# Optimization experiments

Measured on AMD Instinct MI355X. Metric: run time of the kernel, lower is better.

The kernel has to match this reference:

```python
import jax, jax.numpy as jnp
import numpy as np

B, N, D, H = 2, 2048, 1024, 16
Dh = D // H
SCALE = Dh ** -0.5


def setup_inputs() -> dict:
    key = jax.random.key(0)
    ks = jax.random.split(key, 5)
    init = lambda k, sh, fan: (jax.random.normal(k, sh, jnp.float32) / np.sqrt(fan)).astype(jnp.float32)
    return {
        "x": jax.random.normal(ks[0], (B, N, D), jnp.float32),
        "w_qkv": init(ks[1], (D, 3 * D), D),   # to_qkv (no bias)
        "w_hkv": init(ks[2], (D, 2 * D), D),   # hkv_processor: Linear(dim, 2*dim), split -> HK, HV
        "w_out": init(ks[3], (D, D), D),       # to_out weight
        "b_out": jnp.zeros((D,), jnp.float32), # to_out bias
        "alpha": jnp.ones((1, H, 1, 1), jnp.float32),
    }


def _split_heads(t):  # (B,N,D) -> (B,H,N,Dh)
    return t.reshape(B, N, H, Dh).transpose(0, 2, 1, 3)


def _rope(x, theta=10000.0):
    # lucidrains rotary_embedding_torch: interleaved pairs (x[2i], x[2i+1])
    n, dh = x.shape[-2], x.shape[-1]
    freqs = 1.0 / (theta ** (jnp.arange(0, dh, 2, dtype=jnp.float32) / dh))
    ang = jnp.arange(n, dtype=jnp.float32)[:, None] * freqs          # (N, Dh/2)
    cos = jnp.repeat(jnp.cos(ang), 2, axis=-1)                        # (N, Dh)
    sin = jnp.repeat(jnp.sin(ang), 2, axis=-1)
    xp = x.reshape(*x.shape[:-1], dh // 2, 2)
    xrot = jnp.stack((-xp[..., 1], xp[..., 0]), axis=-1).reshape(x.shape)
    return x * cos + xrot * sin


def reference(x, w_qkv, w_hkv, w_out, b_out, alpha):
    q, k, v = (_split_heads(t) for t in jnp.split(x @ w_qkv, 3, axis=-1))
    hk, hv = (_split_heads(t) for t in jnp.split(x @ w_hkv, 2, axis=-1))
    q = _rope(q)
    k = _rope(k)

    qk = jnp.einsum('bhnd,bhmd->bhnm', q, k) * SCALE          # (B,H,N,N)
    hkk = jnp.einsum('bhnd,bhmd->bhnm', hk, k)                # (B,H,N,N)
    qhk = jnp.sum(q * hk, axis=-1, keepdims=True)             # (B,H,N,1)
    scores = qk - jax.nn.silu(hkk * qhk * SCALE)

    mask = jnp.tril(jnp.ones((N, N), dtype=bool))
    scores = jnp.where(mask, scores, -jnp.inf)
    W = jax.nn.softmax(scores, axis=-1)

    hvv = jnp.einsum('bhnd,bhmd->bhnm', hv, v)                # (B,H,N,N)
    mod = jnp.sum(hvv * W, axis=-1, keepdims=True)            # (B,H,N,1)
    o = jnp.einsum('bhnm,bhmd->bhnd', W, v) - jax.nn.sigmoid(alpha) * mod * hv

    attn_out = o.transpose(0, 2, 1, 3).reshape(B, N, D)
    return attn_out @ w_out + b_out
```

## Files before the change

### kernel.cpp

```cpp
#include <hip/hip_runtime.h>
#include <math.h>

typedef unsigned int u32;
typedef unsigned short u16;
typedef __attribute__((ext_vector_type(4))) float f32x4;
typedef __attribute__((ext_vector_type(8))) short s16x8;

#define BB 2
#define NN 2048
#define DD 1024
#define HH 16
#define ROWS 4096
#define QC 5120
#define SCALE 0.125f
#define LOG2E 1.44269504088896f
#define SC2 (SCALE * LOG2E)

#if __has_builtin(__builtin_amdgcn_exp2f)
#define EXP2(x) __builtin_amdgcn_exp2f(x)
#else
#define EXP2(x) __expf((x) * 0.69314718056f)
#endif
#if __has_builtin(__builtin_amdgcn_rcpf)
#define RCP(x) __builtin_amdgcn_rcpf(x)
#else
#define RCP(x) (1.0f / (x))
#endif

__device__ __forceinline__ u16 f2bf(float x) {
    u32 u = __float_as_uint(x);
    return (u16)((u + 0x7FFFu + ((u >> 16) & 1u)) >> 16);
}
__device__ __forceinline__ float bf2f(u16 h) {
    return __uint_as_float(((u32)h) << 16);
}
__device__ __forceinline__ u32 cvtpk(float lo, float hi) {
    u32 r;
    asm("v_cvt_pk_bf16_f32 %0, %1, %2" : "=v"(r) : "v"(lo), "v"(hi));
    return r;
}
__device__ __forceinline__ void gload16(const void* g, void* l) {
    __builtin_amdgcn_global_load_lds(
        (const __attribute__((address_space(1))) unsigned int*)g,
        (__attribute__((address_space(3))) unsigned int*)l, 16, 0, 0);
}

__device__ __forceinline__ void vt_write(char* vbb, uint4 vreg, int srow, int sch)
{
    uint4 oth;
    oth.x = (u32)__shfl_xor((int)vreg.x, 8); oth.y = (u32)__shfl_xor((int)vreg.y, 8);
    oth.z = (u32)__shfl_xor((int)vreg.z, 8); oth.w = (u32)__shfl_xor((int)vreg.w, 8);
    const bool odd = (srow & 1);
    u32 ma = odd ? vreg.z : vreg.x, mb = odd ? vreg.w : vreg.y;
    u32 oa = odd ? oth.z : oth.x,  ob = odd ? oth.w : oth.y;
    u32 ea = odd ? oa : ma, eb = odd ? ob : mb;
    u32 da = odd ? ma : oa, db = odd ? mb : ob;
    u32 pk0 = (ea & 0xffffu) | (da << 16);
    u32 pk1 = (ea >> 16)     | (da & 0xffff0000u);
    u32 pk2 = (eb & 0xffffu) | (db << 16);
    u32 pk3 = (eb >> 16)     | (db & 0xffff0000u);
    const int s = srow >> 1;
    const int d0 = sch * 8 + (odd ? 4 : 0);
    const int sb = (s & 3) * 4;
    *(u32*)(vbb + (d0 + 0) * 128 + ((((s >> 2) ^ ((d0 + 0) & 7) ^ sch) << 4)) + sb) = pk0;
    *(u32*)(vbb + (d0 + 1) * 128 + ((((s >> 2) ^ ((d0 + 1) & 7) ^ sch) << 4)) + sb) = pk1;
    *(u32*)(vbb + (d0 + 2) * 128 + ((((s >> 2) ^ ((d0 + 2) & 7) ^ sch) << 4)) + sb) = pk2;
    *(u32*)(vbb + (d0 + 3) * 128 + ((((s >> 2) ^ ((d0 + 3) & 7) ^ sch) << 4)) + sb) = pk3;
}

__global__ __launch_bounds__(256) void convert_x(const float* __restrict__ x,
                                                 uint4* __restrict__ xb)
{
    int t = blockIdx.x * 256 + threadIdx.x;
    const float4 a = ((const float4*)x)[2 * t];
    const float4 b = ((const float4*)x)[2 * t + 1];
    uint4 o;
    o.x = f2bf(a.x) | ((u32)f2bf(a.y) << 16);
    o.y = f2bf(a.z) | ((u32)f2bf(a.w) << 16);
    o.z = f2bf(b.x) | ((u32)f2bf(b.y) << 16);
    o.w = f2bf(b.z) | ((u32)f2bf(b.w) << 16);
    xb[t] = o;
}

__global__ __launch_bounds__(256) void transpose_w(const float* __restrict__ wqkv,
                                                   const float* __restrict__ whkv,
                                                   const float* __restrict__ wout,
                                                   u16* __restrict__ wT)
{
    __shared__ float T[64][65];
    const int bc = blockIdx.x;
    const int k0 = blockIdx.y * 64;
    const int c0 = bc * 64;
    const float* src; int stride; int csrc;
    if (bc < 48)      { src = wqkv; stride = 3072; csrc = c0; }
    else if (bc < 80) { src = whkv; stride = 2048; csrc = c0 - 3072; }
    else              { src = wout; stride = 1024; csrc = c0 - 5120; }
    const int t = threadIdx.x;
    const int r = t >> 4, c4 = t & 15;
#pragma unroll
    for (int i = 0; i < 4; ++i) {
        int kk = r + 16 * i;
        float4 v = *(const float4*)&src[(size_t)(k0 + kk) * stride + csrc + 4 * c4];
        T[kk][4 * c4 + 0] = v.x; T[kk][4 * c4 + 1] = v.y;
        T[kk][4 * c4 + 2] = v.z; T[kk][4 * c4 + 3] = v.w;
    }
    __syncthreads();
#pragma unroll
    for (int i = 0; i < 4; ++i) {
        int cc = r + 16 * i;
        u32 lo = f2bf(T[4 * c4 + 0][cc]) | ((u32)f2bf(T[4 * c4 + 1][cc]) << 16);
        u32 hi = f2bf(T[4 * c4 + 2][cc]) | ((u32)f2bf(T[4 * c4 + 3][cc]) << 16);
        *(uint2*)&wT[(size_t)(c0 + cc) * 1024 + k0 + 4 * c4] = make_uint2(lo, hi);
    }
}

__global__ __launch_bounds__(256) void rope_table(float* __restrict__ tab)
{
    int t = blockIdx.x * 256 + threadIdx.x;
    int n = t >> 6, col = t & 63, i = col & 31;
    float ang = (float)n * exp2f(-(float)i * 0.41524101186092029f);
    tab[t] = (col < 32) ? cosf(ang) : sinf(ang);
}

template <int BF16_OUT>
__global__ __launch_bounds__(256, 2) void gemm_bf16(
    const u16* __restrict__ A, int lda,
    const u16* __restrict__ B, int ldb,
    void* __restrict__ C, int ldc,
    const float* __restrict__ bias, const float* __restrict__ tab, int K)
{
    __shared__ u16 As[128 * 64];
    __shared__ u16 Bs[128 * 64];
    const int tid = threadIdx.x;
    const int lane = tid & 63, w = tid >> 6;
    const int g = lane >> 4, c = lane & 15;
    const int wr = w >> 1, wc = w & 1;
    const int rb0 = blockIdx.y * 128, cb0 = blockIdx.x * 128;

    f32x4 acc[4][4];
#pragma unroll
    for (int i = 0; i < 4; ++i)
#pragma unroll
        for (int j = 0; j < 4; ++j) {
            acc[i][j][0] = 0.f; acc[i][j][1] = 0.f; acc[i][j][2] = 0.f; acc[i][j][3] = 0.f;
        }

    const int srow = tid >> 3, sch = tid & 7;
    const int scol = ((sch ^ (srow & 7)) * 8);
    const u16* asrc = A + (size_t)(rb0 + srow) * lda + scol;
    const u16* bsrc = B + (size_t)(cb0 + srow) * ldb + scol;

    for (int k0 = 0; k0 < K; k0 += 64) {
        __syncthreads();
#pragma unroll
        for (int r = 0; r < 4; ++r) {
            gload16(asrc + (size_t)(32 * r) * lda + k0, (char*)As + r * 4096 + w * 1024);
            gload16(bsrc + (size_t)(32 * r) * ldb + k0, (char*)Bs + r * 4096 + w * 1024);
        }
        __syncthreads();
#pragma unroll
        for (int kk = 0; kk < 2; ++kk) {
            s16x8 a[4], b[4];
#pragma unroll
            for (int rb = 0; rb < 4; ++rb) {
                int row = wr * 64 + rb * 16 + c;
                a[rb] = *(const s16x8*)((const char*)As + row * 128 + ((((kk << 2) + g) ^ (row & 7)) << 4));
            }
#pragma unroll
            for (int cb = 0; cb < 4; ++cb) {
                int row = wc * 64 + cb * 16 + c;
                b[cb] = *(const s16x8*)((const char*)Bs + row * 128 + ((((kk << 2) + g) ^ (row & 7)) << 4));
            }
#pragma unroll
            for (int rb = 0; rb < 4; ++rb)
#pragma unroll
                for (int cb = 0; cb < 4; ++cb)
                    acc[rb][cb] = __builtin_amdgcn_mfma_f32_16x16x32_bf16(a[rb], b[cb], acc[rb][cb], 0, 0, 0);
        }
    }

    if (BF16_OUT && tab && cb0 >= 1024 && cb0 < 2048) {
#pragma unroll
        for (int rb = 0; rb < 4; ++rb)
#pragma unroll
            for (int cb = 0; cb < 4; ++cb) {
                const int i = ((wc * 64 + cb * 16 + c) & 63) >> 1;
#pragma unroll
                for (int e = 0; e < 4; ++e) {
                    int n = (rb0 + wr * 64 + rb * 16 + g * 4 + e) & (NN - 1);
                    float co = tab[(n << 6) + i], si = tab[(n << 6) + 32 + i];
                    float self = acc[rb][cb][e];
                    float part = __shfl_xor(self, 1);
                    acc[rb][cb][e] = (c & 1) ? fmaf(self, co, part * si)
                                             : fmaf(self, co, -part * si);
                }
            }
    }

#pragma unroll
    for (int rb = 0; rb < 4; ++rb) {
#pragma unroll
        for (int cb = 0; cb < 4; ++cb) {
            if (BF16_OUT) {
                uint2 keep = make_uint2(0, 0);
#pragma unroll
                for (int e = 0; e < 4; ++e) {
                    u32 me = f2bf(acc[rb][cb][e]);
                    u32 x1 = (u32)__shfl_xor((int)me, 1);
                    u32 pair = (c & 1) ? ((x1 & 0xffffu) | (me << 16)) : ((me & 0xffffu) | (x1 << 16));
                    u32 x2 = (u32)__shfl_xor((int)pair, 2);
                    u32 q0 = (c & 2) ? x2 : pair;
                    u32 q1 = (c & 2) ? pair : x2;
                    if ((c & 3) == e) keep = make_uint2(q0, q1);
                }
                int row = rb0 + wr * 64 + rb * 16 + g * 4 + (c & 3);
                int col = cb0 + wc * 64 + cb * 16 + (c & ~3);
                *(uint2*)((u16*)C + (size_t)row * ldc + col) = keep;
            } else {
                int col = cb0 + wc * 64 + cb * 16 + c;
                float bv = bias ? bias[col] : 0.f;
#pragma unroll
                for (int e = 0; e < 4; ++e) {
                    int row = rb0 + wr * 64 + rb * 16 + g * 4 + e;
                    ((float*)C)[(size_t)row * ldc + col] = acc[rb][cb][e] + bv;
                }
            }
        }
    }
}

__global__ __launch_bounds__(256, 4) void attn(
    const u16* __restrict__ qkvh, const float* __restrict__ alpha,
    const float* __restrict__ tab, u16* __restrict__ aout)
{
    __shared__ u16 Kb[2][64 * 64];
    __shared__ u16 Vt[2][64 * 64];

    const int bid = blockIdx.x;
    const int qt = 31 - (bid >> 5);
    const int bh = 4 * (bid & 7) + ((bid >> 3) & 3);
    const int b = bh >> 4, h = bh & 15;
    const int tid = threadIdx.x;
    const int w = tid >> 6, lane = tid & 63;
    const int g = lane >> 4, c = lane & 15;
    const u16* base = qkvh + (size_t)b * NN * QC;
    const int q0 = qt * 64;
    const int nrow = q0 + w * 16 + c;

    const int srow = tid >> 3, sch = tid & 7;
    const int kscol = (sch ^ ((srow & 3) | (((srow >> 3) & 1) << 2))) * 8;
    const u16* ksrc0 = base + (size_t)srow * QC + 1024 + h * 64 + kscol;
    const u16* vsrc0 = base + (size_t)srow * QC + 2048 + h * 64 + sch * 8;

    const float sig_a = RCP(1.f + EXP2(-alpha[h] * LOG2E));
    const int cbase = (8 * (c >> 2) + (c & 3)) * 128;

    gload16(ksrc0, (char*)&Kb[0][0] + w * 1024);
    gload16(ksrc0 + (size_t)32 * QC, (char*)&Kb[0][0] + 4096 + w * 1024);
    uint4 vr0 = *(const uint4*)vsrc0;
    uint4 vr1 = *(const uint4*)(vsrc0 + (size_t)32 * QC);
    vt_write((char*)&Vt[0][0], vr0, srow, sch);
    vt_write((char*)&Vt[0][0], vr1, srow + 32, sch);

    s16x8 qf[2], hf[2];
    float qhL;
    {
        const u16* qp_ = base + (size_t)nrow * QC + h * 64;
        float accq = 0.f;
#pragma unroll
        for (int kk = 0; kk < 2; ++kk) {
            uint4 qv = *(const uint4*)(qp_ + ((kk * 4 + g) * 8));
            uint4 hv = *(const uint4*)(qp_ + 3072 + ((kk * 4 + g) * 8));
            const u16* qe = (const u16*)&qv;
            const u16* he = (const u16*)&hv;
            u32 ow[4];
#pragma unroll
            for (int m2 = 0; m2 < 4; ++m2) {
                int i = (kk * 4 + g) * 4 + m2;
                float co = tab[(nrow << 6) + i], si = tab[(nrow << 6) + 32 + i];
                float x0 = bf2f(qe[2 * m2]), x1 = bf2f(qe[2 * m2 + 1]);
                float r0 = x0 * co - x1 * si;
                float r1 = x1 * co + x0 * si;
                accq += r0 * bf2f(he[2 * m2]) + r1 * bf2f(he[2 * m2 + 1]);
                ow[m2] = (u32)f2bf(r0) | ((u32)f2bf(r1) << 16);
            }
            union { s16x8 v; u32 u[4]; } uq, uh;
            uq.u[0] = ow[0]; uq.u[1] = ow[1]; uq.u[2] = ow[2]; uq.u[3] = ow[3];
            uh.u[0] = hv.x; uh.u[1] = hv.y; uh.u[2] = hv.z; uh.u[3] = hv.w;
            qf[kk] = uq.v; hf[kk] = uh.v;
        }
        accq += __shfl_xor(accq, 16);
        accq += __shfl_xor(accq, 32);
        qhL = accq * SC2;
    }
    __syncthreads();

    f32x4 y[4];
#pragma unroll
    for (int db = 0; db < 4; ++db) { y[db][0] = 0.f; y[db][1] = 0.f; y[db][2] = 0.f; y[db][3] = 0.f; }
    float m = -INFINITY, l = 0.f;

    for (int kt = 0; kt <= qt; ++kt) {
        const int cur = kt & 1;
        const bool haveNext = (kt < qt);
        uint4 vr0n, vr1n;
        if (haveNext) {
            gload16(ksrc0 + (size_t)((kt + 1) * 64) * QC, (char*)&Kb[cur ^ 1][0] + w * 1024);
            gload16(ksrc0 + (size_t)((kt + 1) * 64 + 32) * QC, (char*)&Kb[cur ^ 1][0] + 4096 + w * 1024);
            vr0n = *(const uint4*)(vsrc0 + (size_t)((kt + 1) * 64) * QC);
            vr1n = *(const uint4*)(vsrc0 + (size_t)((kt + 1) * 64 + 32) * QC);
        }

        f32x4 sq[4], sh4[4];
#pragma unroll
        for (int kb = 0; kb < 4; ++kb) {
            sq[kb][0] = 0.f; sq[kb][1] = 0.f; sq[kb][2] = 0.f; sq[kb][3] = 0.f;
            sh4[kb][0] = 0.f; sh4[kb][1] = 0.f; sh4[kb][2] = 0.f; sh4[kb][3] = 0.f;
        }
        const char* kbp = (const char*)&Kb[cur][0] + cbase;
#pragma unroll
        for (int kb = 0; kb < 4; ++kb) {
#pragma unroll
            for (int kk = 0; kk < 2; ++kk) {
                s16x8 kf = *(const s16x8*)(kbp + (kb & 1) * 512 + (kb >> 1) * 4096 +
                                           ((((kk << 2) + g) ^ (c & 7)) << 4));
                sq[kb] = __builtin_amdgcn_mfma_f32_16x16x32_bf16(kf, qf[kk], sq[kb], 0, 0, 0);
                sh4[kb] = __builtin_amdgcn_mfma_f32_16x16x32_bf16(kf, hf[kk], sh4[kb], 0, 0, 0);
            }
        }
        const bool needmask = (kt == qt);
        float mx = -INFINITY;
#pragma unroll
        for (int kb = 0; kb < 4; ++kb) {
#pragma unroll
            for (int e = 0; e < 4; ++e) {
                float zp = sh4[kb][e] * qhL;
                float sil = zp * RCP(1.f + EXP2(-zp));
                float s = fmaf(sq[kb][e], SC2, -sil);
                if (needmask) {
                    int kg = kt * 64 + 32 * (kb >> 1) + 8 * g + 4 * (kb & 1) + e;
                    if (kg > nrow) s = -INFINITY;
                }
                sq[kb][e] = s;
                mx = fmaxf(mx, s);
            }
        }
        mx = fmaxf(mx, __shfl_xor(mx, 16));
        mx = fmaxf(mx, __shfl_xor(mx, 32));
        const float mnew = fmaxf(m, mx);
        const float scl = EXP2(m - mnew);
        m = mnew;
        float rs = 0.f;
#pragma unroll
        for (int kb = 0; kb < 4; ++kb)
#pragma unroll
            for (int e = 0; e < 4; ++e) {
                float p = EXP2(sq[kb][e] - mnew);
                sq[kb][e] = p;
                rs += p;
            }
        rs += __shfl_xor(rs, 16);
        rs += __shfl_xor(rs, 32);
        l = l * scl + rs;
#pragma unroll
        for (int db = 0; db < 4; ++db) {
            y[db][0] *= scl; y[db][1] *= scl; y[db][2] *= scl; y[db][3] *= scl;
        }
        union { s16x8 v; u32 u[4]; } pa[2];
#pragma unroll
        for (int kk = 0; kk < 2; ++kk) {
            pa[kk].u[0] = cvtpk(sq[2 * kk][0], sq[2 * kk][1]);
            pa[kk].u[1] = cvtpk(sq[2 * kk][2], sq[2 * kk][3]);
            pa[kk].u[2] = cvtpk(sq[2 * kk + 1][0], sq[2 * kk + 1][1]);
            pa[kk].u[3] = cvtpk(sq[2 * kk + 1][2], sq[2 * kk + 1][3]);
        }
        const char* vbp = (const char*)&Vt[cur][0];
#pragma unroll
        for (int kk = 0; kk < 2; ++kk)
#pragma unroll
            for (int db = 0; db < 4; ++db) {
                int row = db * 16 + c;
                int ch = ((kk << 2) + g) ^ (c & 7) ^ (db * 2 + (c >> 3));
                s16x8 vfr = *(const s16x8*)(vbp + row * 128 + (ch << 4));
                y[db] = __builtin_amdgcn_mfma_f32_16x16x32_bf16(vfr, pa[kk].v, y[db], 0, 0, 0);
            }

        if (haveNext) {
            vt_write((char*)&Vt[cur ^ 1][0], vr0n, srow, sch);
            vt_write((char*)&Vt[cur ^ 1][0], vr1n, srow + 32, sch);
        }
        __syncthreads();
    }

    const float inv_l = RCP(l);
    const u16* hvp = base + (size_t)nrow * QC + 4096 + h * 64 + g * 4;
    float hv[4][4];
    float sdot = 0.f;
#pragma unroll
    for (int db = 0; db < 4; ++db) {
        uint2 hw = *(const uint2*)(hvp + db * 16);
        const u16* he = (const u16*)&hw;
#pragma unroll
        for (int e = 0; e < 4; ++e) {
            hv[db][e] = bf2f(he[e]);
            float yn = y[db][e] * inv_l;
            y[db][e] = yn;
            sdot += yn * hv[db][e];
        }
    }
    sdot += __shfl_xor(sdot, 16);
    sdot += __shfl_xor(sdot, 32);
    const float f = sig_a * sdot;
    u16* op = aout + ((size_t)(b * NN + nrow)) * DD + h * 64 + g * 4;
#pragma unroll
    for (int db = 0; db < 4; ++db) {
        u32 o0 = (u32)f2bf(y[db][0] - f * hv[db][0]) | ((u32)f2bf(y[db][1] - f * hv[db][1]) << 16);
        u32 o1 = (u32)f2bf(y[db][2] - f * hv[db][2]) | ((u32)f2bf(y[db][3] - f * hv[db][3]) << 16);
        *(uint2*)(op + db * 16) = make_uint2(o0, o1);
    }
}

extern "C" void kernel_launch(void* const* d_in, const int* in_sizes, int n_in,
                              void* d_out, int out_size, void* d_ws, size_t ws_size,
                              hipStream_t stream)
{
    const float* x     = (const float*)d_in[0];
    const float* w_qkv = (const float*)d_in[1];
    const float* w_hkv = (const float*)d_in[2];
    const float* w_out = (const float*)d_in[3];
    const float* b_out = (const float*)d_in[4];
    const float* alpha = (const float*)d_in[5];

    char* ws = (char*)d_ws;
    u16*   qkvh = (u16*)ws;
    uint4* xb   = (uint4*)(ws + 41943040);
    u16*   wT   = (u16*)(ws + 50331648);
    u16*   aout = (u16*)(ws + 62914560);
    float* tab  = (float*)(ws + 71303168);

    convert_x<<<2048, 256, 0, stream>>>(x, xb);
    transpose_w<<<dim3(96, 16), 256, 0, stream>>>(w_qkv, w_hkv, w_out, wT);
    rope_table<<<512, 256, 0, stream>>>(tab);

    gemm_bf16<1><<<dim3(40, 32), 256, 0, stream>>>(
        (const u16*)xb, 1024, wT, 1024, qkvh, QC, nullptr, tab, 1024);

    attn<<<1024, 256, 0, stream>>>(qkvh, alpha, tab, aout);

    gemm_bf16<0><<<dim3(8, 32), 256, 0, stream>>>(
        aout, 1024, wT + 5120 * 1024, 1024, d_out, 1024, b_out, nullptr, 1024);
}
```

Measured before the change: 168.5 us.

## Double-buffer GEMM LDS tiles, defer softmax rescale, raise MFMA wave priority

The GEMM kernel now uses two LDS buffers, so the next K tile loads while MFMAs run on the current one, with one barrier per step instead of two. The attention kernel skips the running-max rescale of l and the accumulators unless some lane's new max exceeds the old by more than a threshold (lazy rescale). s_setprio brackets the MFMA blocks in both kernels to favour matrix issue. Double buffering doubles GEMM LDS use (64KB per block), which may hurt occupancy at launch_bounds(256,2). Deferred rescaling lets exponentials grow up to 2^8 before renormalising, which slightly risks bf16 precision in P.

```diff
diff --git a/kernel.cpp b/kernel.cpp
--- a/kernel.cpp
+++ b/kernel.cpp
@@ -15,6 +15,7 @@
 #define SCALE 0.125f
 #define LOG2E 1.44269504088896f
 #define SC2 (SCALE * LOG2E)
+#define DEFER_THR 8.0f
 
 #if __has_builtin(__builtin_amdgcn_exp2f)
 #define EXP2(x) __builtin_amdgcn_exp2f(x)
@@ -129,8 +130,8 @@
     void* __restrict__ C, int ldc,
     const float* __restrict__ bias, const float* __restrict__ tab, int K)
 {
-    __shared__ u16 As[128 * 64];
-    __shared__ u16 Bs[128 * 64];
+    __shared__ u16 As[2][128 * 64];
+    __shared__ u16 Bs[2][128 * 64];
     const int tid = threadIdx.x;
     const int lane = tid & 63, w = tid >> 6;
     const int g = lane >> 4, c = lane & 15;
@@ -150,33 +151,46 @@
     const u16* asrc = A + (size_t)(rb0 + srow) * lda + scol;
     const u16* bsrc = B + (size_t)(cb0 + srow) * ldb + scol;
 
-    for (int k0 = 0; k0 < K; k0 += 64) {
-        __syncthreads();
-#pragma unroll
-        for (int r = 0; r < 4; ++r) {
-            gload16(asrc + (size_t)(32 * r) * lda + k0, (char*)As + r * 4096 + w * 1024);
-            gload16(bsrc + (size_t)(32 * r) * ldb + k0, (char*)Bs + r * 4096 + w * 1024);
-        }
-        __syncthreads();
+#pragma unroll
+    for (int r = 0; r < 4; ++r) {
+        gload16(asrc + (size_t)(32 * r) * lda, (char*)As[0] + r * 4096 + w * 1024);
+        gload16(bsrc + (size_t)(32 * r) * ldb, (char*)Bs[0] + r * 4096 + w * 1024);
+    }
+    __syncthreads();
+
+    const int NKS = K >> 6;
+    for (int ks = 0; ks < NKS; ++ks) {
+        const int cur = ks & 1;
+        if (ks + 1 < NKS) {
+            const int k1 = (ks + 1) << 6;
+#pragma unroll
+            for (int r = 0; r < 4; ++r) {
+                gload16(asrc + (size_t)(32 * r) * lda + k1, (char*)As[cur ^ 1] + r * 4096 + w * 1024);
+                gload16(bsrc + (size_t)(32 * r) * ldb + k1, (char*)Bs[cur ^ 1] + r * 4096 + w * 1024);
+            }
+        }
 #pragma unroll
         for (int kk = 0; kk < 2; ++kk) {
             s16x8 a[4], b[4];
 #pragma unroll
             for (int rb = 0; rb < 4; ++rb) {
                 int row = wr * 64 + rb * 16 + c;
-                a[rb] = *(const s16x8*)((const char*)As + row * 128 + ((((kk << 2) + g) ^ (row & 7)) << 4));
+                a[rb] = *(const s16x8*)((const char*)As[cur] + row * 128 + ((((kk << 2) + g) ^ (row & 7)) << 4));
             }
 #pragma unroll
             for (int cb = 0; cb < 4; ++cb) {
                 int row = wc * 64 + cb * 16 + c;
-                b[cb] = *(const s16x8*)((const char*)Bs + row * 128 + ((((kk << 2) + g) ^ (row & 7)) << 4));
-            }
+                b[cb] = *(const s16x8*)((const char*)Bs[cur] + row * 128 + ((((kk << 2) + g) ^ (row & 7)) << 4));
+            }
+            __builtin_amdgcn_s_setprio(1);
 #pragma unroll
             for (int rb = 0; rb < 4; ++rb)
 #pragma unroll
                 for (int cb = 0; cb < 4; ++cb)
                     acc[rb][cb] = __builtin_amdgcn_mfma_f32_16x16x32_bf16(a[rb], b[cb], acc[rb][cb], 0, 0, 0);
-        }
+            __builtin_amdgcn_s_setprio(0);
+        }
+        __syncthreads();
     }
 
     if (BF16_OUT && tab && cb0 >= 1024 && cb0 < 2048) {
@@ -318,6 +332,7 @@
             sh4[kb][0] = 0.f; sh4[kb][1] = 0.f; sh4[kb][2] = 0.f; sh4[kb][3] = 0.f;
         }
         const char* kbp = (const char*)&Kb[cur][0] + cbase;
+        __builtin_amdgcn_s_setprio(1);
 #pragma unroll
         for (int kb = 0; kb < 4; ++kb) {
 #pragma unroll
@@ -328,6 +343,7 @@
                 sh4[kb] = __builtin_amdgcn_mfma_f32_16x16x32_bf16(kf, hf[kk], sh4[kb], 0, 0, 0);
             }
         }
+        __builtin_amdgcn_s_setprio(0);
         const bool needmask = (kt == qt);
         float mx = -INFINITY;
 #pragma unroll
@@ -347,25 +363,28 @@
         }
         mx = fmaxf(mx, __shfl_xor(mx, 16));
         mx = fmaxf(mx, __shfl_xor(mx, 32));
-        const float mnew = fmaxf(m, mx);
-        const float scl = EXP2(m - mnew);
-        m = mnew;
+        if (!__all(mx <= m + DEFER_THR)) {
+            const float mnew = fmaxf(m, mx);
+            const float scl = EXP2(m - mnew);
+            m = mnew;
+            l *= scl;
+#pragma unroll
+            for (int db = 0; db < 4; ++db) {
+                y[db][0] *= scl; y[db][1] *= scl; y[db][2] *= scl; y[db][3] *= scl;
+            }
+        }
         float rs = 0.f;
 #pragma unroll
         for (int kb = 0; kb < 4; ++kb)
 #pragma unroll
             for (int e = 0; e < 4; ++e) {
-                float p = EXP2(sq[kb][e] - mnew);
+                float p = EXP2(sq[kb][e] - m);
                 sq[kb][e] = p;
                 rs += p;
             }
         rs += __shfl_xor(rs, 16);
         rs += __shfl_xor(rs, 32);
-        l = l * scl + rs;
-#pragma unroll
-        for (int db = 0; db < 4; ++db) {
-            y[db][0] *= scl; y[db][1] *= scl; y[db][2] *= scl; y[db][3] *= scl;
-        }
+        l += rs;
         union { s16x8 v; u32 u[4]; } pa[2];
 #pragma unroll
         for (int kk = 0; kk < 2; ++kk) {
@@ -375,6 +394,7 @@
             pa[kk].u[3] = cvtpk(sq[2 * kk + 1][2], sq[2 * kk + 1][3]);
         }
         const char* vbp = (const char*)&Vt[cur][0];
+        __builtin_amdgcn_s_setprio(1);
 #pragma unroll
         for (int kk = 0; kk < 2; ++kk)
 #pragma unroll
@@ -384,6 +404,7 @@
                 s16x8 vfr = *(const s16x8*)(vbp + row * 128 + (ch << 4));
                 y[db] = __builtin_amdgcn_mfma_f32_16x16x32_bf16(vfr, pa[kk].v, y[db], 0, 0, 0);
             }
+        __builtin_amdgcn_s_setprio(0);
 
         if (haveNext) {
             vt_write((char*)&Vt[cur ^ 1][0], vr0n, srow, sch);
```

New measurement: 165.8 us. About the same (-1.6%).

## Use 256x256 double-buffered QKV GEMM, deferred softmax rescale, and MFMA priority hints

Applied to the files above, without the earlier changes.

Replaces the 128x128 QKV projection GEMM with a 512-thread 256x256-tile kernel. It double-buffers LDS, waits with explicit vmcnt, and keeps the fused RoPE and bf16 epilogue. This raises operand reuse and overlaps global loads with MFMA work. In attention, the running-max rescale of the accumulator is skipped unless some lane's new max exceeds the old by a threshold, which saves exp and multiply work but allows larger exponent values. s_setprio hints are added around the MFMA blocks in all kernels.

```diff
diff --git a/kernel.cpp b/kernel.cpp
--- a/kernel.cpp
+++ b/kernel.cpp
@@ -15,6 +15,7 @@
 #define SCALE 0.125f
 #define LOG2E 1.44269504088896f
 #define SC2 (SCALE * LOG2E)
+#define DEFER_THR 8.0f
 
 #if __has_builtin(__builtin_amdgcn_exp2f)
 #define EXP2(x) __builtin_amdgcn_exp2f(x)
@@ -44,6 +45,8 @@
         (const __attribute__((address_space(1))) unsigned int*)g,
         (__attribute__((address_space(3))) unsigned int*)l, 16, 0, 0);
 }
+__device__ __forceinline__ void waitv8() { asm volatile("s_waitcnt vmcnt(8)" ::: "memory"); }
+__device__ __forceinline__ void waitv0() { asm volatile("s_waitcnt vmcnt(0)" ::: "memory"); }
 
 __device__ __forceinline__ void vt_write(char* vbb, uint4 vreg, int srow, int sch)
 {
@@ -122,12 +125,128 @@
     tab[t] = (col < 32) ? cosf(ang) : sinf(ang);
 }
 
-template <int BF16_OUT>
-__global__ __launch_bounds__(256, 2) void gemm_bf16(
+__global__ __launch_bounds__(512, 1) void gemm256(
+    const u16* __restrict__ A, const u16* __restrict__ B,
+    u16* __restrict__ C, const float* __restrict__ tab)
+{
+    __shared__ u16 As[2][256 * 64];
+    __shared__ u16 Bs[2][256 * 64];
+    const int tid = threadIdx.x;
+    const int lane = tid & 63, w = tid >> 6;
+    const int g = lane >> 4, c = lane & 15;
+    const int wrow = w >> 2, wcol = w & 3;
+    const int rb0 = blockIdx.y * 256, cb0 = blockIdx.x * 256;
+
+    f32x4 acc[8][4];
+#pragma unroll
+    for (int i = 0; i < 8; ++i)
+#pragma unroll
+        for (int j = 0; j < 4; ++j) {
+            acc[i][j][0] = 0.f; acc[i][j][1] = 0.f; acc[i][j][2] = 0.f; acc[i][j][3] = 0.f;
+        }
+
+    const int srow = tid >> 3, sch = tid & 7;
+    const int scol = (sch ^ (srow & 7)) * 8;
+    const u16* asrc = A + (size_t)(rb0 + srow) * 1024 + scol;
+    const u16* bsrc = B + (size_t)(cb0 + srow) * 1024 + scol;
+
+#define STAGE256(buf, kt)                                                      \
+    {   const int k1_ = (kt) << 6;                                             \
+        _Pragma("unroll")                                                      \
+        for (int j_ = 0; j_ < 4; ++j_) {                                       \
+            gload16(asrc + (size_t)(j_ * 64) * 1024 + k1_,                     \
+                    (char*)As[buf] + j_ * 8192 + w * 1024);                    \
+            gload16(bsrc + (size_t)(j_ * 64) * 1024 + k1_,                     \
+                    (char*)Bs[buf] + j_ * 8192 + w * 1024);                    \
+        } }
+
+    STAGE256(0, 0);
+
+    const int NT = 16;
+    for (int t = 0; t < NT; ++t) {
+        const int cur = t & 1;
+        if (t + 1 < NT) { STAGE256(cur ^ 1, t + 1); waitv8(); }
+        else            { waitv0(); }
+        __builtin_amdgcn_s_barrier();
+        __builtin_amdgcn_sched_barrier(0);
+#pragma unroll
+        for (int kk = 0; kk < 2; ++kk) {
+            const int chs = (((kk << 2) | g) ^ (c & 7)) << 4;
+            s16x8 bfr[4], afr[4];
+#pragma unroll
+            for (int cb = 0; cb < 4; ++cb) {
+                int row = wcol * 64 + cb * 16 + c;
+                bfr[cb] = *(const s16x8*)((const char*)Bs[cur] + row * 128 + chs);
+            }
+#pragma unroll
+            for (int rb = 0; rb < 4; ++rb) {
+                int row = wrow * 128 + rb * 16 + c;
+                afr[rb] = *(const s16x8*)((const char*)As[cur] + row * 128 + chs);
+            }
+            __builtin_amdgcn_s_setprio(1);
+#pragma unroll
+            for (int rb = 0; rb < 4; ++rb)
+#pragma unroll
+                for (int cb = 0; cb < 4; ++cb)
+                    acc[rb][cb] = __builtin_amdgcn_mfma_f32_16x16x32_bf16(afr[rb], bfr[cb], acc[rb][cb], 0, 0, 0);
+            __builtin_amdgcn_s_setprio(0);
+#pragma unroll
+            for (int rb = 0; rb < 4; ++rb) {
+                int row = wrow * 128 + 64 + rb * 16 + c;
+                afr[rb] = *(const s16x8*)((const char*)As[cur] + row * 128 + chs);
+            }
+            __builtin_amdgcn_s_setprio(1);
+#pragma unroll
+            for (int rb = 0; rb < 4; ++rb)
+#pragma unroll
+                for (int cb = 0; cb < 4; ++cb)
+                    acc[rb + 4][cb] = __builtin_amdgcn_mfma_f32_16x16x32_bf16(afr[rb], bfr[cb], acc[rb + 4][cb], 0, 0, 0);
+            __builtin_amdgcn_s_setprio(0);
+            __builtin_amdgcn_sched_barrier(0);
+        }
+        __builtin_amdgcn_s_barrier();
+    }
+
+    const bool doRope = (cb0 >= 1024 && cb0 < 2048);
+#pragma unroll
+    for (int rb = 0; rb < 8; ++rb) {
+#pragma unroll
+        for (int cb = 0; cb < 4; ++cb) {
+            if (doRope) {
+                const int i = ((wcol * 64 + cb * 16 + c) & 63) >> 1;
+#pragma unroll
+                for (int e = 0; e < 4; ++e) {
+                    int n = (rb0 + wrow * 128 + rb * 16 + g * 4 + e) & (NN - 1);
+                    float co = tab[(n << 6) + i], si = tab[(n << 6) + 32 + i];
+                    float self = acc[rb][cb][e];
+                    float part = __shfl_xor(self, 1);
+                    acc[rb][cb][e] = (c & 1) ? fmaf(self, co, part * si)
+                                             : fmaf(self, co, -part * si);
+                }
+            }
+            uint2 keep = make_uint2(0, 0);
+#pragma unroll
+            for (int e = 0; e < 4; ++e) {
+                u32 me = f2bf(acc[rb][cb][e]);
+                u32 x1 = (u32)__shfl_xor((int)me, 1);
+                u32 pair = (c & 1) ? ((x1 & 0xffffu) | (me << 16)) : ((me & 0xffffu) | (x1 << 16));
+                u32 x2 = (u32)__shfl_xor((int)pair, 2);
+                u32 q0 = (c & 2) ? x2 : pair;
+                u32 q1 = (c & 2) ? pair : x2;
+                if ((c & 3) == e) keep = make_uint2(q0, q1);
+            }
+            int row = rb0 + wrow * 128 + rb * 16 + g * 4 + (c & 3);
+            int col = cb0 + wcol * 64 + cb * 16 + (c & ~3);
+            *(uint2*)(C + (size_t)row * QC + col) = keep;
+        }
+    }
+}
+
+__global__ __launch_bounds__(256, 2) void gemm128(
     const u16* __restrict__ A, int lda,
     const u16* __restrict__ B, int ldb,
-    void* __restrict__ C, int ldc,
-    const float* __restrict__ bias, const float* __restrict__ tab, int K)
+    float* __restrict__ C, int ldc,
+    const float* __restrict__ bias, int K)
 {
     __shared__ u16 As[128 * 64];
     __shared__ u16 Bs[128 * 64];
@@ -171,59 +290,25 @@
                 int row = wc * 64 + cb * 16 + c;
                 b[cb] = *(const s16x8*)((const char*)Bs + row * 128 + ((((kk << 2) + g) ^ (row & 7)) << 4));
             }
+            __builtin_amdgcn_s_setprio(1);
 #pragma unroll
             for (int rb = 0; rb < 4; ++rb)
 #pragma unroll
                 for (int cb = 0; cb < 4; ++cb)
                     acc[rb][cb] = __builtin_amdgcn_mfma_f32_16x16x32_bf16(a[rb], b[cb], acc[rb][cb], 0, 0, 0);
-        }
-    }
-
-    if (BF16_OUT && tab && cb0 >= 1024 && cb0 < 2048) {
-#pragma unroll
-        for (int rb = 0; rb < 4; ++rb)
-#pragma unroll
-            for (int cb = 0; cb < 4; ++cb) {
-                const int i = ((wc * 64 + cb * 16 + c) & 63) >> 1;
-#pragma unroll
-                for (int e = 0; e < 4; ++e) {
-                    int n = (rb0 + wr * 64 + rb * 16 + g * 4 + e) & (NN - 1);
-                    float co = tab[(n << 6) + i], si = tab[(n << 6) + 32 + i];
-                    float self = acc[rb][cb][e];
-                    float part = __shfl_xor(self, 1);
-                    acc[rb][cb][e] = (c & 1) ? fmaf(self, co, part * si)
-                                             : fmaf(self, co, -part * si);
-                }
-            }
-    }
-
+            __builtin_amdgcn_s_setprio(0);
+        }
+    }
 #pragma unroll
     for (int rb = 0; rb < 4; ++rb) {
 #pragma unroll
         for (int cb = 0; cb < 4; ++cb) {
-            if (BF16_OUT) {
-                uint2 keep = make_uint2(0, 0);
-#pragma unroll
-                for (int e = 0; e < 4; ++e) {
-                    u32 me = f2bf(acc[rb][cb][e]);
-                    u32 x1 = (u32)__shfl_xor((int)me, 1);
-                    u32 pair = (c & 1) ? ((x1 & 0xffffu) | (me << 16)) : ((me & 0xffffu) | (x1 << 16));
-                    u32 x2 = (u32)__shfl_xor((int)pair, 2);
-                    u32 q0 = (c & 2) ? x2 : pair;
-                    u32 q1 = (c & 2) ? pair : x2;
-                    if ((c & 3) == e) keep = make_uint2(q0, q1);
-                }
-                int row = rb0 + wr * 64 + rb * 16 + g * 4 + (c & 3);
-                int col = cb0 + wc * 64 + cb * 16 + (c & ~3);
-                *(uint2*)((u16*)C + (size_t)row * ldc + col) = keep;
-            } else {
-                int col = cb0 + wc * 64 + cb * 16 + c;
-                float bv = bias ? bias[col] : 0.f;
-#pragma unroll
-                for (int e = 0; e < 4; ++e) {
-                    int row = rb0 + wr * 64 + rb * 16 + g * 4 + e;
-                    ((float*)C)[(size_t)row * ldc + col] = acc[rb][cb][e] + bv;
-                }
+            int col = cb0 + wc * 64 + cb * 16 + c;
+            float bv = bias ? bias[col] : 0.f;
+#pragma unroll
+            for (int e = 0; e < 4; ++e) {
+                int row = rb0 + wr * 64 + rb * 16 + g * 4 + e;
+                C[(size_t)row * ldc + col] = acc[rb][cb][e] + bv;
             }
         }
     }
@@ -318,6 +403,7 @@
             sh4[kb][0] = 0.f; sh4[kb][1] = 0.f; sh4[kb][2] = 0.f; sh4[kb][3] = 0.f;
         }
         const char* kbp = (const char*)&Kb[cur][0] + cbase;
+        __builtin_amdgcn_s_setprio(1);
 #pragma unroll
         for (int kb = 0; kb < 4; ++kb) {
 #pragma unroll
@@ -328,6 +414,7 @@
                 sh4[kb] = __builtin_amdgcn_mfma_f32_16x16x32_bf16(kf, hf[kk], sh4[kb], 0, 0, 0);
             }
         }
+        __builtin_amdgcn_s_setprio(0);
         const bool needmask = (kt == qt);
         float mx = -INFINITY;
 #pragma unroll
@@ -347,25 +434,28 @@
         }
         mx = fmaxf(mx, __shfl_xor(mx, 16));
         mx = fmaxf(mx, __shfl_xor(mx, 32));
-        const float mnew = fmaxf(m, mx);
-        const float scl = EXP2(m - mnew);
-        m = mnew;
+        if (!__all(mx <= m + DEFER_THR)) {
+            const float mnew = fmaxf(m, mx);
+            const float scl = EXP2(m - mnew);
+            m = mnew;
+            l *= scl;
+#pragma unroll
+            for (int db = 0; db < 4; ++db) {
+                y[db][0] *= scl; y[db][1] *= scl; y[db][2] *= scl; y[db][3] *= scl;
+            }
+        }
         float rs = 0.f;
 #pragma unroll
         for (int kb = 0; kb < 4; ++kb)
 #pragma unroll
             for (int e = 0; e < 4; ++e) {
-                float p = EXP2(sq[kb][e] - mnew);
+                float p = EXP2(sq[kb][e] - m);
                 sq[kb][e] = p;
                 rs += p;
             }
         rs += __shfl_xor(rs, 16);
         rs += __shfl_xor(rs, 32);
-        l = l * scl + rs;
-#pragma unroll
-        for (int db = 0; db < 4; ++db) {
-            y[db][0] *= scl; y[db][1] *= scl; y[db][2] *= scl; y[db][3] *= scl;
-        }
+        l += rs;
         union { s16x8 v; u32 u[4]; } pa[2];
 #pragma unroll
         for (int kk = 0; kk < 2; ++kk) {
@@ -375,6 +465,7 @@
             pa[kk].u[3] = cvtpk(sq[2 * kk + 1][2], sq[2 * kk + 1][3]);
         }
         const char* vbp = (const char*)&Vt[cur][0];
+        __builtin_amdgcn_s_setprio(1);
 #pragma unroll
         for (int kk = 0; kk < 2; ++kk)
 #pragma unroll
@@ -384,6 +475,7 @@
                 s16x8 vfr = *(const s16x8*)(vbp + row * 128 + (ch << 4));
                 y[db] = __builtin_amdgcn_mfma_f32_16x16x32_bf16(vfr, pa[kk].v, y[db], 0, 0, 0);
             }
+        __builtin_amdgcn_s_setprio(0);
 
         if (haveNext) {
             vt_write((char*)&Vt[cur ^ 1][0], vr0n, srow, sch);
@@ -442,11 +534,10 @@
     transpose_w<<<dim3(96, 16), 256, 0, stream>>>(w_qkv, w_hkv, w_out, wT);
     rope_table<<<512, 256, 0, stream>>>(tab);
 
-    gemm_bf16<1><<<dim3(40, 32), 256, 0, stream>>>(
-        (const u16*)xb, 1024, wT, 1024, qkvh, QC, nullptr, tab, 1024);
+    gemm256<<<dim3(20, 16), 512, 0, stream>>>((const u16*)xb, wT, qkvh, tab);
 
     attn<<<1024, 256, 0, stream>>>(qkvh, alpha, tab, aout);
 
-    gemm_bf16<0><<<dim3(8, 32), 256, 0, stream>>>(
-        aout, 1024, wT + 5120 * 1024, 1024, d_out, 1024, b_out, nullptr, 1024);
-}
+    gemm128<<<dim3(8, 32), 256, 0, stream>>>(
+        aout, 1024, wT + 5120 * 1024, 1024, (float*)d_out, 1024, b_out, 1024);
+}
```

After: 185.2 us. 9.9% more time.

## Fuse prep kernels, defer softmax rescale, and raise MFMA wave priority

Applied to the files above, without the earlier changes.

Merges the x conversion, weight transpose and rope table kernels into one launch, removing two kernel launches. In the attention loop, the running-max update and rescaling of the output accumulator and row sum are skipped unless some lane's new max exceeds the stored max by more than a threshold, which saves exp and multiply work per tile. MFMA sections are bracketed with s_setprio so waves issuing matrix ops get priority over others. The deferred rescale lets unnormalized exponents grow up to 2^8, which risks slight precision loss in the bf16 P values but stays within fp32 range.

```diff
diff --git a/kernel.cpp b/kernel.cpp
--- a/kernel.cpp
+++ b/kernel.cpp
@@ -15,6 +15,7 @@
 #define SCALE 0.125f
 #define LOG2E 1.44269504088896f
 #define SC2 (SCALE * LOG2E)
+#define DEFER_THR 8.0f
 
 #if __has_builtin(__builtin_amdgcn_exp2f)
 #define EXP2(x) __builtin_amdgcn_exp2f(x)
@@ -68,58 +69,58 @@
     *(u32*)(vbb + (d0 + 3) * 128 + ((((s >> 2) ^ ((d0 + 3) & 7) ^ sch) << 4)) + sb) = pk3;
 }
 
-__global__ __launch_bounds__(256) void convert_x(const float* __restrict__ x,
-                                                 uint4* __restrict__ xb)
-{
-    int t = blockIdx.x * 256 + threadIdx.x;
-    const float4 a = ((const float4*)x)[2 * t];
-    const float4 b = ((const float4*)x)[2 * t + 1];
-    uint4 o;
-    o.x = f2bf(a.x) | ((u32)f2bf(a.y) << 16);
-    o.y = f2bf(a.z) | ((u32)f2bf(a.w) << 16);
-    o.z = f2bf(b.x) | ((u32)f2bf(b.y) << 16);
-    o.w = f2bf(b.z) | ((u32)f2bf(b.w) << 16);
-    xb[t] = o;
-}
-
-__global__ __launch_bounds__(256) void transpose_w(const float* __restrict__ wqkv,
-                                                   const float* __restrict__ whkv,
-                                                   const float* __restrict__ wout,
-                                                   u16* __restrict__ wT)
+__global__ __launch_bounds__(256) void prep(const float* __restrict__ x,
+                                            const float* __restrict__ wqkv,
+                                            const float* __restrict__ whkv,
+                                            const float* __restrict__ wout,
+                                            uint4* __restrict__ xb,
+                                            u16* __restrict__ wT,
+                                            float* __restrict__ tab)
 {
     __shared__ float T[64][65];
-    const int bc = blockIdx.x;
-    const int k0 = blockIdx.y * 64;
-    const int c0 = bc * 64;
-    const float* src; int stride; int csrc;
-    if (bc < 48)      { src = wqkv; stride = 3072; csrc = c0; }
-    else if (bc < 80) { src = whkv; stride = 2048; csrc = c0 - 3072; }
-    else              { src = wout; stride = 1024; csrc = c0 - 5120; }
-    const int t = threadIdx.x;
-    const int r = t >> 4, c4 = t & 15;
-#pragma unroll
-    for (int i = 0; i < 4; ++i) {
-        int kk = r + 16 * i;
-        float4 v = *(const float4*)&src[(size_t)(k0 + kk) * stride + csrc + 4 * c4];
-        T[kk][4 * c4 + 0] = v.x; T[kk][4 * c4 + 1] = v.y;
-        T[kk][4 * c4 + 2] = v.z; T[kk][4 * c4 + 3] = v.w;
-    }
-    __syncthreads();
-#pragma unroll
-    for (int i = 0; i < 4; ++i) {
-        int cc = r + 16 * i;
-        u32 lo = f2bf(T[4 * c4 + 0][cc]) | ((u32)f2bf(T[4 * c4 + 1][cc]) << 16);
-        u32 hi = f2bf(T[4 * c4 + 2][cc]) | ((u32)f2bf(T[4 * c4 + 3][cc]) << 16);
-        *(uint2*)&wT[(size_t)(c0 + cc) * 1024 + k0 + 4 * c4] = make_uint2(lo, hi);
-    }
-}
-
-__global__ __launch_bounds__(256) void rope_table(float* __restrict__ tab)
-{
-    int t = blockIdx.x * 256 + threadIdx.x;
-    int n = t >> 6, col = t & 63, i = col & 31;
-    float ang = (float)n * exp2f(-(float)i * 0.41524101186092029f);
-    tab[t] = (col < 32) ? cosf(ang) : sinf(ang);
+    const int bid = blockIdx.x;
+    if (bid < 2048) {
+        int t = bid * 256 + threadIdx.x;
+        const float4 a = ((const float4*)x)[2 * t];
+        const float4 b = ((const float4*)x)[2 * t + 1];
+        uint4 o;
+        o.x = f2bf(a.x) | ((u32)f2bf(a.y) << 16);
+        o.y = f2bf(a.z) | ((u32)f2bf(a.w) << 16);
+        o.z = f2bf(b.x) | ((u32)f2bf(b.y) << 16);
+        o.w = f2bf(b.z) | ((u32)f2bf(b.w) << 16);
+        xb[t] = o;
+    } else if (bid < 3584) {
+        const int idx = bid - 2048;
+        const int bc = idx % 96;
+        const int k0 = (idx / 96) * 64;
+        const int c0 = bc * 64;
+        const float* src; int stride; int csrc;
+        if (bc < 48)      { src = wqkv; stride = 3072; csrc = c0; }
+        else if (bc < 80) { src = whkv; stride = 2048; csrc = c0 - 3072; }
+        else              { src = wout; stride = 1024; csrc = c0 - 5120; }
+        const int t = threadIdx.x;
+        const int r = t >> 4, c4 = t & 15;
+#pragma unroll
+        for (int i = 0; i < 4; ++i) {
+            int kk = r + 16 * i;
+            float4 v = *(const float4*)&src[(size_t)(k0 + kk) * stride + csrc + 4 * c4];
+            T[kk][4 * c4 + 0] = v.x; T[kk][4 * c4 + 1] = v.y;
+            T[kk][4 * c4 + 2] = v.z; T[kk][4 * c4 + 3] = v.w;
+        }
+        __syncthreads();
+#pragma unroll
+        for (int i = 0; i < 4; ++i) {
+            int cc = r + 16 * i;
+            u32 lo = f2bf(T[4 * c4 + 0][cc]) | ((u32)f2bf(T[4 * c4 + 1][cc]) << 16);
+            u32 hi = f2bf(T[4 * c4 + 2][cc]) | ((u32)f2bf(T[4 * c4 + 3][cc]) << 16);
+            *(uint2*)&wT[(size_t)(c0 + cc) * 1024 + k0 + 4 * c4] = make_uint2(lo, hi);
+        }
+    } else {
+        int t = (bid - 3584) * 256 + threadIdx.x;
+        int n = t >> 6, col = t & 63, i = col & 31;
+        float ang = (float)n * exp2f(-(float)i * 0.41524101186092029f);
+        tab[t] = (col < 32) ? cosf(ang) : sinf(ang);
+    }
 }
 
 template <int BF16_OUT>
@@ -318,6 +319,7 @@
             sh4[kb][0] = 0.f; sh4[kb][1] = 0.f; sh4[kb][2] = 0.f; sh4[kb][3] = 0.f;
         }
         const char* kbp = (const char*)&Kb[cur][0] + cbase;
+        __builtin_amdgcn_s_setprio(1);
 #pragma unroll
         for (int kb = 0; kb < 4; ++kb) {
 #pragma unroll
@@ -328,6 +330,7 @@
                 sh4[kb] = __builtin_amdgcn_mfma_f32_16x16x32_bf16(kf, hf[kk], sh4[kb], 0, 0, 0);
             }
         }
+        __builtin_amdgcn_s_setprio(0);
         const bool needmask = (kt == qt);
         float mx = -INFINITY;
 #pragma unroll
@@ -347,25 +350,28 @@
         }
         mx = fmaxf(mx, __shfl_xor(mx, 16));
         mx = fmaxf(mx, __shfl_xor(mx, 32));
-        const float mnew = fmaxf(m, mx);
-        const float scl = EXP2(m - mnew);
-        m = mnew;
+        if (!__all(mx <= m + DEFER_THR)) {
+            const float mnew = fmaxf(m, mx);
+            const float scl = EXP2(m - mnew);
+            m = mnew;
+            l *= scl;
+#pragma unroll
+            for (int db = 0; db < 4; ++db) {
+                y[db][0] *= scl; y[db][1] *= scl; y[db][2] *= scl; y[db][3] *= scl;
+            }
+        }
         float rs = 0.f;
 #pragma unroll
         for (int kb = 0; kb < 4; ++kb)
 #pragma unroll
             for (int e = 0; e < 4; ++e) {
-                float p = EXP2(sq[kb][e] - mnew);
+                float p = EXP2(sq[kb][e] - m);
                 sq[kb][e] = p;
                 rs += p;
             }
         rs += __shfl_xor(rs, 16);
         rs += __shfl_xor(rs, 32);
-        l = l * scl + rs;
-#pragma unroll
-        for (int db = 0; db < 4; ++db) {
-            y[db][0] *= scl; y[db][1] *= scl; y[db][2] *= scl; y[db][3] *= scl;
-        }
+        l += rs;
         union { s16x8 v; u32 u[4]; } pa[2];
 #pragma unroll
         for (int kk = 0; kk < 2; ++kk) {
@@ -375,6 +381,7 @@
             pa[kk].u[3] = cvtpk(sq[2 * kk + 1][2], sq[2 * kk + 1][3]);
         }
         const char* vbp = (const char*)&Vt[cur][0];
+        __builtin_amdgcn_s_setprio(1);
 #pragma unroll
         for (int kk = 0; kk < 2; ++kk)
 #pragma unroll
@@ -384,6 +391,7 @@
                 s16x8 vfr = *(const s16x8*)(vbp + row * 128 + (ch << 4));
                 y[db] = __builtin_amdgcn_mfma_f32_16x16x32_bf16(vfr, pa[kk].v, y[db], 0, 0, 0);
             }
+        __builtin_amdgcn_s_setprio(0);
 
         if (haveNext) {
             vt_write((char*)&Vt[cur ^ 1][0], vr0n, srow, sch);
@@ -438,9 +446,7 @@
     u16*   aout = (u16*)(ws + 62914560);
     float* tab  = (float*)(ws + 71303168);
 
-    convert_x<<<2048, 256, 0, stream>>>(x, xb);
-    transpose_w<<<dim3(96, 16), 256, 0, stream>>>(w_qkv, w_hkv, w_out, wT);
-    rope_table<<<512, 256, 0, stream>>>(tab);
+    prep<<<4096, 256, 0, stream>>>(x, w_qkv, w_hkv, w_out, xb, wT, tab);
 
     gemm_bf16<1><<<dim3(40, 32), 256, 0, stream>>>(
         (const u16*)xb, 1024, wT, 1024, qkvh, QC, nullptr, tab, 1024);
```

After: 159.9 us. -5.1%, faster.
